# Performance work log

Hardware: AMD Instinct MI355X
Metric: run time of the kernel (lower is better)

## Reference

```python
import jax, jax.numpy as jnp
import numpy as np

# Ragged layout: 8 sequences packed into total_tokens=6144 tokens.
_SEQLENS = [1024, 512, 1024, 256, 768, 1024, 512, 1024]
_TOTAL = sum(_SEQLENS)  # 6144
_H, _D = 16, 128
_MAXLEN = 1024


def setup_inputs() -> dict:
    key = jax.random.key(0)
    kq, kk, kv = jax.random.split(key, 3)
    cu = jnp.asarray(np.concatenate([[0], np.cumsum(_SEQLENS)]), dtype=jnp.int32)
    return {
        "q": jax.random.normal(kq, (_TOTAL, _H, _D), dtype=jnp.float32),
        "k": jax.random.normal(kk, (_TOTAL, _H, _D), dtype=jnp.float32),
        "v": jax.random.normal(kv, (_TOTAL, _H, _D), dtype=jnp.float32),
        "cu_seqlens_q": cu,
        "cu_seqlens_k": cu,
        "max_seqlen_q": _MAXLEN,
        "max_seqlen_k": _MAXLEN,
    }


def _pad_gather(x, cu, L):
    """Gather packed [T,h,d] into padded [B,L,h,d] plus validity mask [B,L]."""
    starts = cu[:-1]                                   # [B]
    lens = cu[1:] - cu[:-1]                            # [B]
    pos = jnp.arange(L, dtype=cu.dtype)                # [L]
    idx = starts[:, None] + pos[None, :]               # [B,L]
    mask = pos[None, :] < lens[:, None]                # [B,L]
    idx = jnp.clip(idx, 0, x.shape[0] - 1)
    return x[idx], mask, jnp.where(mask, idx, x.shape[0])


def reference(q, k, v, cu_seqlens_q, cu_seqlens_k, max_seqlen_q, max_seqlen_k):
    # Equivalent to pytorch_varlen_attention: per-sequence SDPA (non-causal,
    # no dropout), vectorized via pad-to-max + key masking.
    T, h, d = q.shape
    qp, mq, idx_q = _pad_gather(q, cu_seqlens_q, max_seqlen_q)  # [B,Lq,h,d]
    kp, mk, _ = _pad_gather(k, cu_seqlens_k, max_seqlen_k)      # [B,Lk,h,d]
    vp, _, _ = _pad_gather(v, cu_seqlens_k, max_seqlen_k)

    scale = 1.0 / jnp.sqrt(jnp.asarray(d, dtype=q.dtype))
    scores = jnp.einsum("bqhd,bkhd->bhqk", qp, kp) * scale      # [B,h,Lq,Lk]
    neg = jnp.asarray(jnp.finfo(scores.dtype).min, scores.dtype)
    scores = jnp.where(mk[:, None, None, :], scores, neg)
    attn = jax.nn.softmax(scores, axis=-1)
    out_pad = jnp.einsum("bhqk,bkhd->bqhd", attn, vp)           # [B,Lq,h,d]

    # Scatter valid rows back to packed layout; invalid rows dropped (idx==T).
    out = jnp.zeros((T, h, d), dtype=q.dtype)
    out = out.at[idx_q.reshape(-1)].set(
        out_pad.reshape(-1, h, d), mode="drop")
    return out
```

## Files before the change

### kernel.cpp

```cpp
#include <hip/hip_runtime.h>
#include <hip/hip_bf16.h>
#include <stdint.h>

#define H 16
#define D 128
#define BM 256
#define BN 64
#define NW 8
#define NT 512

typedef __bf16 bf16_t;
typedef bf16_t bf16x8 __attribute__((ext_vector_type(8)));
typedef bf16_t bf16x2 __attribute__((ext_vector_type(2)));
typedef float f32x16 __attribute__((ext_vector_type(16)));

#define MFMA32(a, b, c) __builtin_amdgcn_mfma_f32_32x32x16_bf16(a, b, c, 0, 0, 0)

union FragU { uint32_t w[4]; bf16x8 v; };

static __device__ __forceinline__ uint32_t cvtpk_bf16(float lo, float hi) {
  uint32_t r;
  asm("v_cvt_pk_bf16_f32 %0, %1, %2" : "=v"(r) : "v"(lo), "v"(hi));
  return r;
}

static __device__ __forceinline__ void gld_lds16(const bf16_t* g, bf16_t* l) {
  __builtin_amdgcn_global_load_lds(
      (const __attribute__((address_space(1))) void*)g,
      (__attribute__((address_space(3))) void*)l, 16, 0, 0);
}

static __device__ __forceinline__ float xhalf(float v, int hi) {
  uint32_t b = __builtin_bit_cast(uint32_t, v);
  auto p = __builtin_amdgcn_permlane32_swap(b, b, false, false);
  uint32_t o = hi ? p[0] : p[1];
  return __builtin_bit_cast(float, o);
}


__global__ void conv_k(const float* __restrict__ kin, bf16_t* __restrict__ kb, int n8) {
  int i = blockIdx.x * blockDim.x + threadIdx.x;
  int stride = gridDim.x * blockDim.x;
  for (; i < n8; i += stride) {
    const float* p = kin + (size_t)i * 8;
    float4 a = *(const float4*)p, b = *(const float4*)(p + 4);
    bf16x8 w;
    w[0] = (bf16_t)a.x; w[1] = (bf16_t)a.y; w[2] = (bf16_t)a.z; w[3] = (bf16_t)a.w;
    w[4] = (bf16_t)b.x; w[5] = (bf16_t)b.y; w[6] = (bf16_t)b.z; w[7] = (bf16_t)b.w;
    *(bf16x8*)(kb + (size_t)i * 8) = w;
  }
}

__global__ void conv_vt(const float* __restrict__ v, bf16_t* __restrict__ vt,
                        const int* __restrict__ cuk, int nseq) {
  int tile = blockIdx.x, h = blockIdx.y;
  int acc = 0, seq = -1, lt = 0, s0k = 0, Lk = 0, Lkp = 0;
  size_t vb = 0;
  for (int s = 0; s < nseq; ++s) {
    int Ls = cuk[s + 1] - cuk[s];
    int Lp = (Ls + 63) & ~63;
    int nt = Lp / 64;
    if (tile < acc + nt) { seq = s; lt = tile - acc; s0k = cuk[s]; Lk = Ls; Lkp = Lp; break; }
    acc += nt; vb += (size_t)H * D * Lp;
  }
  if (seq < 0) return;
  int kv0 = lt * 64;
  int d = threadIdx.x;
  bf16x8 w[8];
  #pragma unroll
  for (int j = 0; j < 64; ++j) {
    int kv = kv0 + j;
    int kvc = kv < Lk ? kv : Lk - 1;
    float val = v[((size_t)(s0k + kvc) * H + h) * D + d];
    w[j >> 3][j & 7] = (bf16_t)val;
  }
  bf16_t* dstT = vt + vb + (size_t)h * D * Lkp + (size_t)lt * 8192;
  #pragma unroll
  for (int c = 0; c < 8; ++c)
    *(bf16x8*)(dstT + ((size_t)c * 128 + d) * 8) = w[c];
}


__global__ __launch_bounds__(NT, 2)
void fa_varlen15(const float* __restrict__ q,
                 const bf16_t* __restrict__ kb,
                 const bf16_t* __restrict__ vt,
                 const int* __restrict__ cuq,
                 const int* __restrict__ cuk,
                 float* __restrict__ out,
                 int nseq, int maxtiles)
{
  __shared__ alignas(16) bf16_t sK[2][BN * D];
  __shared__ alignas(16) bf16_t sVt[3][8 * 128 * 8];

  const int nwg = gridDim.x;
  const int orig = blockIdx.x;
  const int qq = nwg >> 3, rr = nwg & 7;
  const int xcd = orig & 7;
  const int wgid = (xcd < rr ? xcd * (qq + 1) : rr * (qq + 1) + (xcd - rr) * qq) + (orig >> 3);
  const int tile = wgid % maxtiles;
  const int h = wgid / maxtiles;

  int acc = 0, seq = -1, lt = 0, s0q = 0, s0k = 0, Lq = 0, Lk = 0, Lkp = 0;
  size_t vb = 0;
  for (int s = 0; s < nseq; ++s) {
    int a = cuq[s], b = cuq[s + 1];
    int Ls = b - a;
    int nt = (Ls + BM - 1) / BM;
    int Lks = cuk[s + 1] - cuk[s];
    int Lp = (Lks + 63) & ~63;
    if (tile < acc + nt) {
      seq = s; lt = tile - acc; s0q = a; Lq = Ls;
      s0k = cuk[s]; Lk = Lks; Lkp = Lp;
      break;
    }
    acc += nt; vb += (size_t)H * D * Lp;
  }
  if (seq < 0) return;

  const int q0 = lt * BM;
  const int tid = threadIdx.x;
  const int lane = tid & 63;
  const int lq = lane & 31;
  const int hi = lane >> 5;

  const float SC = 0.08838834764831845f * 1.44269504088896340f;

  bf16x8 qf[8];
  {
    int warp = tid >> 6;
    int qrow = q0 + warp * 32 + lq; if (qrow >= Lq) qrow = Lq - 1;
    const float* qp = q + ((size_t)(s0q + qrow) * H + h) * D;
    #pragma unroll
    for (int ks = 0; ks < 8; ++ks) {
      const float* p = qp + ks * 16 + hi * 8;
      float4 a = *(const float4*)p, b = *(const float4*)(p + 4);
      bf16x8 r;
      r[0] = (bf16_t)(a.x * SC); r[1] = (bf16_t)(a.y * SC);
      r[2] = (bf16_t)(a.z * SC); r[3] = (bf16_t)(a.w * SC);
      r[4] = (bf16_t)(b.x * SC); r[5] = (bf16_t)(b.y * SC);
      r[6] = (bf16_t)(b.z * SC); r[7] = (bf16_t)(b.w * SC);
      qf[ks] = r;
    }
  }

  const bf16_t* vsrcH = vt + vb + (size_t)h * D * Lkp;

  auto STAGE_K = [&](int tt, int buf) {
    const int kvb = tt * BN;
    #pragma unroll
    for (int i = 0; i < 2; ++i) {
      int g = tid + i * NT;
      int row = g >> 4, cc = g & 15;
      int kvr = kvb + row; if (kvr >= Lk) kvr = Lk - 1;
      const bf16_t* src = kb + ((size_t)(s0k + kvr) * H + h) * D + ((cc ^ (row & 7)) << 3);
      gld_lds16(src, &sK[buf][g * 8]);
    }
  };
  auto STAGE_V = [&](int tt, int buf) {
    const bf16_t* vsrc = vsrcH + (size_t)tt * 8192;
    #pragma unroll
    for (int i = 0; i < 2; ++i) {
      int g = tid + i * NT;
      gld_lds16(vsrc + (size_t)g * 8, &sVt[buf][g * 8]);
    }
  };

  f32x16 oacc[4];
  #pragma unroll
  for (int dt = 0; dt < 4; ++dt)
    #pragma unroll
    for (int r = 0; r < 16; ++r) oacc[dt][r] = 0.f;
  float m = -1e30f, l = 0.f;

  FragU paP, pbP;
  #pragma unroll
  for (int i = 0; i < 4; ++i) { paP.w[i] = 0u; pbP.w[i] = 0u; }
  float alphaP = 1.0f;
  int tP = 0, ctP = 0;

  const int nkv = (Lk + BN - 1) / BN;

  STAGE_K(0, 0);
  STAGE_V(0, 0);
  asm volatile("s_waitcnt vmcnt(0)" ::: "memory");
  __builtin_amdgcn_s_barrier();
  __builtin_amdgcn_sched_barrier(0);

  for (int t = 0; t < nkv; ++t) {
    const int kvb = t * BN;
    int tn = t + 1 < nkv ? t + 1 : nkv - 1;
    STAGE_K(tn, (t + 1) & 1);
    STAGE_V(tn, (t + 1) % 3);

    const bf16_t* sKc = sK[t & 1];
    const bool tail = (kvb + BN > Lk);

    #pragma unroll
    for (int ct = 0; ct < 2; ++ct) {
      f32x16 sa, sb;
      #pragma unroll
      for (int r = 0; r < 16; ++r) { sa[r] = 0.f; sb[r] = 0.f; }
      int krow = ct * 32 + lq;
      __builtin_amdgcn_s_setprio(1);
      #pragma unroll
      for (int ks = 0; ks < 4; ++ks) {
        int posa = (ks * 2 + hi) ^ (krow & 7);
        bf16x8 kfa = *(const bf16x8*)&sKc[krow * 128 + (posa << 3)];
        sa = MFMA32(kfa, qf[ks], sa);
        int posb = ((ks + 4) * 2 + hi) ^ (krow & 7);
        bf16x8 kfb = *(const bf16x8*)&sKc[krow * 128 + (posb << 3)];
        sb = MFMA32(kfb, qf[ks + 4], sb);
      }
      __builtin_amdgcn_s_setprio(0);

      if (__any(alphaP != 1.0f)) {
        #pragma unroll
        for (int r = 0; r < 16; ++r) {
          int cr = (r & 3) + 8 * (r >> 2) + 4 * hi;
          float a2 = __shfl(alphaP, cr);
          #pragma unroll
          for (int dt = 0; dt < 4; ++dt) oacc[dt][r] *= a2;
        }
      }
      {
        const bf16_t* sVp = sVt[tP % 3];
        #pragma unroll
        for (int dt = 0; dt < 4; ++dt) {
          int drow = dt * 32 + lq;
          bf16x8 vf0 = *(const bf16x8*)&sVp[((ctP * 4 + hi) * 128 + drow) << 3];
          oacc[dt] = MFMA32(paP.v, vf0, oacc[dt]);
          bf16x8 vf1 = *(const bf16x8*)&sVp[((ctP * 4 + 2 + hi) * 128 + drow) << 3];
          oacc[dt] = MFMA32(pbP.v, vf1, oacc[dt]);
        }
      }

      f32x16 st;
      #pragma unroll
      for (int r = 0; r < 16; ++r) {
        float x = sa[r] + sb[r];
        if (tail) {
          int kvi = kvb + ct * 32 + (r & 3) + 8 * (r >> 2) + 4 * hi;
          if (kvi >= Lk) x = -1e30f;
        }
        st[r] = x;
      }
      float m0;
      {
        float a0 = fmaxf(st[0], st[1]),  a1 = fmaxf(st[2], st[3]);
        float a2 = fmaxf(st[4], st[5]),  a3 = fmaxf(st[6], st[7]);
        float a4 = fmaxf(st[8], st[9]),  a5 = fmaxf(st[10], st[11]);
        float a6 = fmaxf(st[12], st[13]), a7 = fmaxf(st[14], st[15]);
        float b0 = fmaxf(a0, a1), b1 = fmaxf(a2, a3);
        float b2 = fmaxf(a4, a5), b3 = fmaxf(a6, a7);
        m0 = fmaxf(fmaxf(b0, b1), fmaxf(b2, b3));
      }
      float m1 = fmaxf(m0, xhalf(m0, hi));
      bool trig = m1 > m + 8.0f;
      float mnew = trig ? m1 : m;
      float alpha = __builtin_amdgcn_exp2f(m - mnew);
      m = mnew;

      #pragma unroll
      for (int r = 0; r < 16; ++r)
        st[r] = __builtin_amdgcn_exp2f(st[r] - m);
      float psum;
      {
        float a0 = st[0] + st[1],  a1 = st[2] + st[3];
        float a2 = st[4] + st[5],  a3 = st[6] + st[7];
        float a4 = st[8] + st[9],  a5 = st[10] + st[11];
        float a6 = st[12] + st[13], a7 = st[14] + st[15];
        float b0 = a0 + a1, b1 = a2 + a3, b2 = a4 + a5, b3 = a6 + a7;
        psum = (b0 + b1) + (b2 + b3);
      }
      psum += xhalf(psum, hi);
      l = l * alpha + psum;

      uint32_t c0 = cvtpk_bf16(st[0],  st[1]),  c1 = cvtpk_bf16(st[2],  st[3]);
      uint32_t c2 = cvtpk_bf16(st[4],  st[5]),  c3 = cvtpk_bf16(st[6],  st[7]);
      uint32_t c4 = cvtpk_bf16(st[8],  st[9]),  c5 = cvtpk_bf16(st[10], st[11]);
      uint32_t c6 = cvtpk_bf16(st[12], st[13]), c7 = cvtpk_bf16(st[14], st[15]);
      { auto rr2 = __builtin_amdgcn_permlane32_swap(c0, c2, false, false); c0 = rr2[0]; c2 = rr2[1]; }
      { auto rr2 = __builtin_amdgcn_permlane32_swap(c1, c3, false, false); c1 = rr2[0]; c3 = rr2[1]; }
      { auto rr2 = __builtin_amdgcn_permlane32_swap(c4, c6, false, false); c4 = rr2[0]; c6 = rr2[1]; }
      { auto rr2 = __builtin_amdgcn_permlane32_swap(c5, c7, false, false); c5 = rr2[0]; c7 = rr2[1]; }
      paP.w[0] = c0; paP.w[1] = c1; paP.w[2] = c2; paP.w[3] = c3;
      pbP.w[0] = c4; pbP.w[1] = c5; pbP.w[2] = c6; pbP.w[3] = c7;
      alphaP = alpha; tP = t; ctP = ct;
    }

    asm volatile("s_waitcnt vmcnt(2)" ::: "memory");
    __builtin_amdgcn_s_barrier();
    __builtin_amdgcn_sched_barrier(0);
  }

  if (__any(alphaP != 1.0f)) {
    #pragma unroll
    for (int r = 0; r < 16; ++r) {
      int cr = (r & 3) + 8 * (r >> 2) + 4 * hi;
      float a2 = __shfl(alphaP, cr);
      #pragma unroll
      for (int dt = 0; dt < 4; ++dt) oacc[dt][r] *= a2;
    }
  }
  {
    const bf16_t* sVp = sVt[tP % 3];
    #pragma unroll
    for (int dt = 0; dt < 4; ++dt) {
      int drow = dt * 32 + lq;
      bf16x8 vf0 = *(const bf16x8*)&sVp[((ctP * 4 + hi) * 128 + drow) << 3];
      oacc[dt] = MFMA32(paP.v, vf0, oacc[dt]);
      bf16x8 vf1 = *(const bf16x8*)&sVp[((ctP * 4 + 2 + hi) * 128 + drow) << 3];
      oacc[dt] = MFMA32(pbP.v, vf1, oacc[dt]);
    }
  }

  #pragma unroll
  for (int r = 0; r < 16; ++r) {
    int cr = (r & 3) + 8 * (r >> 2) + 4 * hi;
    int warp = tid >> 6;
    int qr = q0 + warp * 32 + cr;
    float lcr = __shfl(l, cr);
    if (qr < Lq) {
      float rn = 1.0f / lcr;
      float* op = out + ((size_t)(s0q + qr) * H + h) * D + lq;
      #pragma unroll
      for (int dt = 0; dt < 4; ++dt)
        op[dt * 32] = oacc[dt][r] * rn;
    }
  }
}


__global__ __launch_bounds__(256, 3)
void fa_varlen2(const float* __restrict__ q,
                const float* __restrict__ k,
                const float* __restrict__ v,
                const int* __restrict__ cuq,
                const int* __restrict__ cuk,
                float* __restrict__ out,
                int nseq)
{
  __shared__ alignas(16) bf16_t sBuf[128 * 128];
  __shared__ float sRed[4 * 32];
  bf16_t* sK  = sBuf;
  bf16_t* sVt = sBuf + 64 * 128;

  const int tile = blockIdx.x;
  const int h = blockIdx.y;

  int acc = 0, seq = -1, lt = 0, s0q = 0, s0k = 0, Lq = 0, Lk = 0;
  for (int s = 0; s < nseq; ++s) {
    int a = cuq[s], b = cuq[s + 1];
    int Ls = b - a;
    int nt = (Ls + 127) / 128;
    if (tile < acc + nt) {
      seq = s; lt = tile - acc; s0q = a; Lq = Ls;
      s0k = cuk[s]; Lk = cuk[s + 1] - s0k;
      break;
    }
    acc += nt;
  }
  if (seq < 0) return;

  const int q0 = lt * 128;
  const int tid = threadIdx.x;
  const int warp = tid >> 6;
  const int lane = tid & 63;
  const int lq = lane & 31;
  const int hi = lane >> 5;

  const float SC = 0.08838834764831845f * 1.44269504088896340f;

  #pragma unroll
  for (int ii = 0; ii < 8; ++ii) {
    int g = tid + ii * 256;
    int row = g >> 4, cc = g & 15;
    int gr = q0 + row; if (gr >= Lq) gr = Lq - 1;
    const float* p = q + ((size_t)(s0q + gr) * H + h) * D + cc * 8;
    float4 f0 = *(const float4*)p;
    float4 f1 = *(const float4*)(p + 4);
    bf16x8 w;
    w[0] = (bf16_t)f0.x; w[1] = (bf16_t)f0.y; w[2] = (bf16_t)f0.z; w[3] = (bf16_t)f0.w;
    w[4] = (bf16_t)f1.x; w[5] = (bf16_t)f1.y; w[6] = (bf16_t)f1.z; w[7] = (bf16_t)f1.w;
    *(bf16x8*)&sBuf[row * 128 + (((cc ^ (row & 7))) << 3)] = w;
  }
  __syncthreads();

  bf16x8 qf[8];
  {
    int row = warp * 32 + lq;
    #pragma unroll
    for (int ks = 0; ks < 8; ++ks) {
      int pos = (ks * 2 + hi) ^ (row & 7);
      qf[ks] = *(const bf16x8*)&sBuf[row * 128 + (pos << 3)];
    }
  }

  f32x16 oacc[4];
  #pragma unroll
  for (int dt = 0; dt < 4; ++dt)
    #pragma unroll
    for (int r = 0; r < 16; ++r) oacc[dt][r] = 0.f;
  float m = -1e30f, l = 0.f;

  const int nkv = (Lk + 63) / 64;
  for (int it = 0; it < nkv; ++it) {
    const int kv0 = it * 64;
    __syncthreads();

    #pragma unroll
    for (int ii = 0; ii < 4; ++ii) {
      int g = tid + ii * 256;
      int row = g >> 4, cc = g & 15;
      int gr = kv0 + row; if (gr >= Lk) gr = Lk - 1;
      const float* p = k + ((size_t)(s0k + gr) * H + h) * D + cc * 8;
      float4 f0 = *(const float4*)p;
      float4 f1 = *(const float4*)(p + 4);
      bf16x8 w;
      w[0] = (bf16_t)f0.x; w[1] = (bf16_t)f0.y; w[2] = (bf16_t)f0.z; w[3] = (bf16_t)f0.w;
      w[4] = (bf16_t)f1.x; w[5] = (bf16_t)f1.y; w[6] = (bf16_t)f1.z; w[7] = (bf16_t)f1.w;
      *(bf16x8*)&sK[row * 128 + (((cc ^ (row & 7))) << 3)] = w;
    }
    {
      int kp = tid & 31;
      int seg = tid >> 5;
      int r0 = kv0 + 2 * kp, r1 = r0 + 1;
      if (r0 >= Lk) r0 = Lk - 1;
      if (r1 >= Lk) r1 = Lk - 1;
      const float* p0 = v + ((size_t)(s0k + r0) * H + h) * D + seg * 16;
      const float* p1 = v + ((size_t)(s0k + r1) * H + h) * D + seg * 16;
      float va[16], vbf[16];
      *(float4*)&va[0]  = *(const float4*)p0;
      *(float4*)&va[4]  = *(const float4*)(p0 + 4);
      *(float4*)&va[8]  = *(const float4*)(p0 + 8);
      *(float4*)&va[12] = *(const float4*)(p0 + 12);
      *(float4*)&vbf[0]  = *(const float4*)p1;
      *(float4*)&vbf[4]  = *(const float4*)(p1 + 4);
      *(float4*)&vbf[8]  = *(const float4*)(p1 + 8);
      *(float4*)&vbf[12] = *(const float4*)(p1 + 12);
      int kvr = 2 * kp;
      #pragma unroll
      for (int i = 0; i < 16; ++i) {
        int d = seg * 16 + i;
        int pos = (kp >> 2) ^ (d & 7);
        bf16x2 w2; w2[0] = (bf16_t)va[i]; w2[1] = (bf16_t)vbf[i];
        *(bf16x2*)&sVt[d * 64 + (pos << 3) + (kvr & 7)] = w2;
      }
    }
    __syncthreads();

    const bool tail = (kv0 + 64 > Lk);

    #pragma unroll
    for (int ct = 0; ct < 2; ++ct) {
      f32x16 st;
      #pragma unroll
      for (int r = 0; r < 16; ++r) st[r] = 0.f;
      int krow = ct * 32 + lq;
      #pragma unroll
      for (int ks = 0; ks < 8; ++ks) {
        int pos = (ks * 2 + hi) ^ (krow & 7);
        bf16x8 kf = *(const bf16x8*)&sK[krow * 128 + (pos << 3)];
        st = MFMA32(kf, qf[ks], st);
      }

      float tmax = -1e30f;
      #pragma unroll
      for (int r = 0; r < 16; ++r) {
        float x = st[r] * SC;
        if (tail) {
          int kvi = kv0 + ct * 32 + (r & 3) + 8 * (r >> 2) + 4 * hi;
          if (kvi >= Lk) x = -1e30f;
        }
        st[r] = x;
        tmax = fmaxf(tmax, x);
      }
      tmax = fmaxf(tmax, __shfl_xor(tmax, 32));
      bool trig = tmax > m + 8.0f;
      float mnew = trig ? tmax : m;
      float alpha = exp2f(m - mnew);
      m = mnew;

      float psum = 0.f;
      #pragma unroll
      for (int r = 0; r < 16; ++r) {
        float e = exp2f(st[r] - m);
        st[r] = e;
        psum += e;
      }
      psum += __shfl_xor(psum, 32);
      l = l * alpha + psum;

      if (__any(alpha != 1.0f)) {
        if (hi == 0) sRed[warp * 32 + lq] = alpha;
        asm volatile("s_waitcnt lgkmcnt(0)" ::: "memory");
        #pragma unroll
        for (int r = 0; r < 16; ++r) {
          float a2 = sRed[warp * 32 + (r & 3) + 8 * (r >> 2) + 4 * hi];
          #pragma unroll
          for (int dt = 0; dt < 4; ++dt) oacc[dt][r] *= a2;
        }
      }

      uint32_t c0 = cvtpk_bf16(st[0],  st[1]),  c1 = cvtpk_bf16(st[2],  st[3]);
      uint32_t c2 = cvtpk_bf16(st[4],  st[5]),  c3 = cvtpk_bf16(st[6],  st[7]);
      uint32_t c4 = cvtpk_bf16(st[8],  st[9]),  c5 = cvtpk_bf16(st[10], st[11]);
      uint32_t c6 = cvtpk_bf16(st[12], st[13]), c7 = cvtpk_bf16(st[14], st[15]);
      { auto rr2 = __builtin_amdgcn_permlane32_swap(c0, c2, false, false); c0 = rr2[0]; c2 = rr2[1]; }
      { auto rr2 = __builtin_amdgcn_permlane32_swap(c1, c3, false, false); c1 = rr2[0]; c3 = rr2[1]; }
      { auto rr2 = __builtin_amdgcn_permlane32_swap(c4, c6, false, false); c4 = rr2[0]; c6 = rr2[1]; }
      { auto rr2 = __builtin_amdgcn_permlane32_swap(c5, c7, false, false); c5 = rr2[0]; c7 = rr2[1]; }
      FragU pa, pb;
      pa.w[0] = c0; pa.w[1] = c1; pa.w[2] = c2; pa.w[3] = c3;
      pb.w[0] = c4; pb.w[1] = c5; pb.w[2] = c6; pb.w[3] = c7;

      #pragma unroll
      for (int dt = 0; dt < 4; ++dt) {
        int drow = dt * 32 + lq;
        int pos0 = (ct * 4 + hi) ^ (drow & 7);
        bf16x8 vf0 = *(const bf16x8*)&sVt[drow * 64 + (pos0 << 3)];
        oacc[dt] = MFMA32(pa.v, vf0, oacc[dt]);
        int pos1 = (ct * 4 + 2 + hi) ^ (drow & 7);
        bf16x8 vf1 = *(const bf16x8*)&sVt[drow * 64 + (pos1 << 3)];
        oacc[dt] = MFMA32(pb.v, vf1, oacc[dt]);
      }
    }
  }

  if (hi == 0) sRed[warp * 32 + lq] = l;
  asm volatile("s_waitcnt lgkmcnt(0)" ::: "memory");
  #pragma unroll
  for (int r = 0; r < 16; ++r) {
    int cr = (r & 3) + 8 * (r >> 2) + 4 * hi;
    int qr = q0 + warp * 32 + cr;
    if (qr < Lq) {
      float rn = 1.0f / sRed[warp * 32 + cr];
      float* op = out + ((size_t)(s0q + qr) * H + h) * D + lq;
      #pragma unroll
      for (int dt = 0; dt < 4; ++dt)
        op[dt * 32] = oacc[dt][r] * rn;
    }
  }
}

extern "C" void kernel_launch(void* const* d_in, const int* in_sizes, int n_in,
                              void* d_out, int out_size, void* d_ws, size_t ws_size,
                              hipStream_t stream) {
  const float* q = (const float*)d_in[0];
  const float* k = (const float*)d_in[1];
  const float* v = (const float*)d_in[2];
  const int* cuq = (const int*)d_in[3];
  const int* cuk = (const int*)d_in[4];
  float* out = (float*)d_out;

  int total = in_sizes[0] / (H * D);
  int nseq = in_sizes[3] - 1;
  int maxtiles = (total + BM - 1) / BM + nseq;

  size_t needK = (size_t)in_sizes[1] * 2;
  size_t needV = (size_t)in_sizes[2] * 2 + (size_t)nseq * 64 * H * D * 2 + 256;

  if (ws_size >= needK + needV) {
    bf16_t* kb = (bf16_t*)d_ws;
    bf16_t* vtb = (bf16_t*)((char*)d_ws + needK);

    conv_k<<<1024, 256, 0, stream>>>(k, kb, in_sizes[1] / 8);
    int maxvt = (total + 63) / 64 + nseq;
    dim3 gvt(maxvt, H);
    conv_vt<<<gvt, 128, 0, stream>>>(v, vtb, cuk, nseq);
    fa_varlen15<<<dim3(maxtiles * H), NT, 0, stream>>>(q, kb, vtb, cuq, cuk, out, nseq, maxtiles);
  } else {
    int mt2 = (total + 127) / 128 + nseq;
    dim3 grid(mt2, H);
    fa_varlen2<<<grid, 256, 0, stream>>>(q, k, v, cuq, cuk, out, nseq);
  }
}
```

Before: 122.4 us.

## Split long-sequence KV range into two chunks with a combine kernel

Adds a split-KV attention kernel. Q tiles of sequences with more than 8 KV tiles are processed by two workgroups, each covering half of the KV range and writing partial outputs plus row max and sum to workspace. A separate combine kernel then merges the two halves. This gives more workgroups and better load balance across CUs for the ragged batch. The cost is an extra launch, bf16 partial-output traffic with some precision loss, and a larger workspace requirement. The old fp32-input fallback kernel is removed.

```diff
diff --git a/kernel.cpp b/kernel.cpp
--- a/kernel.cpp
+++ b/kernel.cpp
@@ -6,12 +6,10 @@
 #define D 128
 #define BM 256
 #define BN 64
-#define NW 8
 #define NT 512
 
 typedef __bf16 bf16_t;
 typedef bf16_t bf16x8 __attribute__((ext_vector_type(8)));
-typedef bf16_t bf16x2 __attribute__((ext_vector_type(2)));
 typedef float f32x16 __attribute__((ext_vector_type(16)));
 
 #define MFMA32(a, b, c) __builtin_amdgcn_mfma_f32_32x32x16_bf16(a, b, c, 0, 0, 0)
@@ -78,6 +76,344 @@
   #pragma unroll
   for (int c = 0; c < 8; ++c)
     *(bf16x8*)(dstT + ((size_t)c * 128 + d) * 8) = w[c];
+}
+
+
+__global__ __launch_bounds__(NT, 2)
+void fa_split(const float* __restrict__ q,
+              const bf16_t* __restrict__ kb,
+              const bf16_t* __restrict__ vt,
+              const int* __restrict__ cuq,
+              const int* __restrict__ cuk,
+              float* __restrict__ out,
+              bf16_t* __restrict__ pO,
+              float* __restrict__ pm,
+              float* __restrict__ pl,
+              int nseq, int maxt, int upb)
+{
+  __shared__ alignas(16) bf16_t sK[2][BN * D];
+  __shared__ alignas(16) bf16_t sVt[3][8 * 128 * 8];
+
+  const int nwg = gridDim.x;
+  const int orig = blockIdx.x;
+  const int qq = nwg >> 3, rr = nwg & 7;
+  const int xcd = orig & 7;
+  const int wgid = (xcd < rr ? xcd * (qq + 1) : rr * (qq + 1) + (xcd - rr) * qq) + (orig >> 3);
+  const int u = wgid % upb;
+  const int h = wgid / upb;
+
+  int accU = 0, accT = 0, seq = -1, qtile = 0, chunk = 0, tileIdx = 0;
+  int s0q = 0, s0k = 0, Lq = 0, Lk = 0, Lkp = 0, nkv = 0, cs = 1;
+  size_t vb = 0;
+  for (int s = 0; s < nseq; ++s) {
+    int a = cuq[s], b = cuq[s + 1];
+    int Ls = b - a;
+    int nt = (Ls + BM - 1) / BM;
+    int Lks = cuk[s + 1] - cuk[s];
+    int Lp = (Lks + 63) & ~63;
+    int nk = (Lks + 63) / 64;
+    int c2 = nk > 8 ? 2 : 1;
+    if (u < accU + nt * c2) {
+      int local = u - accU;
+      seq = s; chunk = local / nt; qtile = local % nt; tileIdx = accT + qtile;
+      s0q = a; Lq = Ls; s0k = cuk[s]; Lk = Lks; Lkp = Lp; nkv = nk; cs = c2;
+      break;
+    }
+    accU += nt * c2; accT += nt; vb += (size_t)H * D * Lp;
+  }
+  if (seq < 0) return;
+
+  const int t0 = chunk * 8;
+  const int t1 = (chunk == 0) ? (nkv < 8 ? nkv : 8) : nkv;
+
+  const int q0 = qtile * BM;
+  const int tid = threadIdx.x;
+  const int lane = tid & 63;
+  const int lq = lane & 31;
+  const int hi = lane >> 5;
+  const int warp = tid >> 6;
+
+  const float SC = 0.08838834764831845f * 1.44269504088896340f;
+
+  bf16x8 qf[8];
+  {
+    int qrow = q0 + warp * 32 + lq; if (qrow >= Lq) qrow = Lq - 1;
+    const float* qp = q + ((size_t)(s0q + qrow) * H + h) * D;
+    #pragma unroll
+    for (int ks = 0; ks < 8; ++ks) {
+      const float* p = qp + ks * 16 + hi * 8;
+      float4 a = *(const float4*)p, b = *(const float4*)(p + 4);
+      bf16x8 r;
+      r[0] = (bf16_t)(a.x * SC); r[1] = (bf16_t)(a.y * SC);
+      r[2] = (bf16_t)(a.z * SC); r[3] = (bf16_t)(a.w * SC);
+      r[4] = (bf16_t)(b.x * SC); r[5] = (bf16_t)(b.y * SC);
+      r[6] = (bf16_t)(b.z * SC); r[7] = (bf16_t)(b.w * SC);
+      qf[ks] = r;
+    }
+  }
+
+  const bf16_t* vsrcH = vt + vb + (size_t)h * D * Lkp;
+
+  auto STAGE_K = [&](int tt, int buf) {
+    const int kvb = tt * BN;
+    #pragma unroll
+    for (int i = 0; i < 2; ++i) {
+      int g = tid + i * NT;
+      int row = g >> 4, cc = g & 15;
+      int kvr = kvb + row; if (kvr >= Lk) kvr = Lk - 1;
+      const bf16_t* src = kb + ((size_t)(s0k + kvr) * H + h) * D + ((cc ^ (row & 7)) << 3);
+      gld_lds16(src, &sK[buf][g * 8]);
+    }
+  };
+  auto STAGE_V = [&](int tt, int buf) {
+    const bf16_t* vsrc = vsrcH + (size_t)tt * 8192;
+    #pragma unroll
+    for (int i = 0; i < 2; ++i) {
+      int g = tid + i * NT;
+      gld_lds16(vsrc + (size_t)g * 8, &sVt[buf][g * 8]);
+    }
+  };
+
+  f32x16 oacc[4];
+  #pragma unroll
+  for (int dt = 0; dt < 4; ++dt)
+    #pragma unroll
+    for (int r = 0; r < 16; ++r) oacc[dt][r] = 0.f;
+  float m = -1e30f, l = 0.f;
+
+  FragU paP, pbP;
+  #pragma unroll
+  for (int i = 0; i < 4; ++i) { paP.w[i] = 0u; pbP.w[i] = 0u; }
+  float alphaP = 1.0f;
+  int tP = t0, ctP = 0;
+
+  STAGE_K(t0, t0 & 1);
+  STAGE_V(t0, t0 % 3);
+  asm volatile("s_waitcnt vmcnt(0)" ::: "memory");
+  __builtin_amdgcn_s_barrier();
+  __builtin_amdgcn_sched_barrier(0);
+
+  for (int t = t0; t < t1; ++t) {
+    const int kvb = t * BN;
+    int tn = t + 1 < t1 ? t + 1 : t1 - 1;
+    STAGE_K(tn, (t + 1) & 1);
+    STAGE_V(tn, (t + 1) % 3);
+
+    const bf16_t* sKc = sK[t & 1];
+    const bool tail = (kvb + BN > Lk);
+
+    #pragma unroll
+    for (int ct = 0; ct < 2; ++ct) {
+      f32x16 sa, sb;
+      #pragma unroll
+      for (int r = 0; r < 16; ++r) { sa[r] = 0.f; sb[r] = 0.f; }
+      int krow = ct * 32 + lq;
+      __builtin_amdgcn_s_setprio(1);
+      #pragma unroll
+      for (int ks = 0; ks < 4; ++ks) {
+        int posa = (ks * 2 + hi) ^ (krow & 7);
+        bf16x8 kfa = *(const bf16x8*)&sKc[krow * 128 + (posa << 3)];
+        sa = MFMA32(kfa, qf[ks], sa);
+        int posb = ((ks + 4) * 2 + hi) ^ (krow & 7);
+        bf16x8 kfb = *(const bf16x8*)&sKc[krow * 128 + (posb << 3)];
+        sb = MFMA32(kfb, qf[ks + 4], sb);
+      }
+      __builtin_amdgcn_s_setprio(0);
+
+      if (__any(alphaP != 1.0f)) {
+        #pragma unroll
+        for (int r = 0; r < 16; ++r) {
+          int cr = (r & 3) + 8 * (r >> 2) + 4 * hi;
+          float a2 = __shfl(alphaP, cr);
+          #pragma unroll
+          for (int dt = 0; dt < 4; ++dt) oacc[dt][r] *= a2;
+        }
+      }
+      {
+        const bf16_t* sVp = sVt[tP % 3];
+        #pragma unroll
+        for (int dt = 0; dt < 4; ++dt) {
+          int drow = dt * 32 + lq;
+          bf16x8 vf0 = *(const bf16x8*)&sVp[((ctP * 4 + hi) * 128 + drow) << 3];
+          oacc[dt] = MFMA32(paP.v, vf0, oacc[dt]);
+          bf16x8 vf1 = *(const bf16x8*)&sVp[((ctP * 4 + 2 + hi) * 128 + drow) << 3];
+          oacc[dt] = MFMA32(pbP.v, vf1, oacc[dt]);
+        }
+      }
+
+      f32x16 st;
+      #pragma unroll
+      for (int r = 0; r < 16; ++r) {
+        float x = sa[r] + sb[r];
+        if (tail) {
+          int kvi = kvb + ct * 32 + (r & 3) + 8 * (r >> 2) + 4 * hi;
+          if (kvi >= Lk) x = -1e30f;
+        }
+        st[r] = x;
+      }
+      float m0;
+      {
+        float a0 = fmaxf(st[0], st[1]),  a1 = fmaxf(st[2], st[3]);
+        float a2 = fmaxf(st[4], st[5]),  a3 = fmaxf(st[6], st[7]);
+        float a4 = fmaxf(st[8], st[9]),  a5 = fmaxf(st[10], st[11]);
+        float a6 = fmaxf(st[12], st[13]), a7 = fmaxf(st[14], st[15]);
+        float b0 = fmaxf(a0, a1), b1 = fmaxf(a2, a3);
+        float b2 = fmaxf(a4, a5), b3 = fmaxf(a6, a7);
+        m0 = fmaxf(fmaxf(b0, b1), fmaxf(b2, b3));
+      }
+      float m1 = fmaxf(m0, xhalf(m0, hi));
+      bool trig = m1 > m + 8.0f;
+      float mnew = trig ? m1 : m;
+      float alpha = __builtin_amdgcn_exp2f(m - mnew);
+      m = mnew;
+
+      #pragma unroll
+      for (int r = 0; r < 16; ++r)
+        st[r] = __builtin_amdgcn_exp2f(st[r] - m);
+      float psum;
+      {
+        float a0 = st[0] + st[1],  a1 = st[2] + st[3];
+        float a2 = st[4] + st[5],  a3 = st[6] + st[7];
+        float a4 = st[8] + st[9],  a5 = st[10] + st[11];
+        float a6 = st[12] + st[13], a7 = st[14] + st[15];
+        float b0 = a0 + a1, b1 = a2 + a3, b2 = a4 + a5, b3 = a6 + a7;
+        psum = (b0 + b1) + (b2 + b3);
+      }
+      psum += xhalf(psum, hi);
+      l = l * alpha + psum;
+
+      uint32_t c0 = cvtpk_bf16(st[0],  st[1]),  c1 = cvtpk_bf16(st[2],  st[3]);
+      uint32_t c2 = cvtpk_bf16(st[4],  st[5]),  c3 = cvtpk_bf16(st[6],  st[7]);
+      uint32_t c4 = cvtpk_bf16(st[8],  st[9]),  c5 = cvtpk_bf16(st[10], st[11]);
+      uint32_t c6 = cvtpk_bf16(st[12], st[13]), c7 = cvtpk_bf16(st[14], st[15]);
+      { auto w2 = __builtin_amdgcn_permlane32_swap(c0, c2, false, false); c0 = w2[0]; c2 = w2[1]; }
+      { auto w2 = __builtin_amdgcn_permlane32_swap(c1, c3, false, false); c1 = w2[0]; c3 = w2[1]; }
+      { auto w2 = __builtin_amdgcn_permlane32_swap(c4, c6, false, false); c4 = w2[0]; c6 = w2[1]; }
+      { auto w2 = __builtin_amdgcn_permlane32_swap(c5, c7, false, false); c5 = w2[0]; c7 = w2[1]; }
+      paP.w[0] = c0; paP.w[1] = c1; paP.w[2] = c2; paP.w[3] = c3;
+      pbP.w[0] = c4; pbP.w[1] = c5; pbP.w[2] = c6; pbP.w[3] = c7;
+      alphaP = alpha; tP = t; ctP = ct;
+    }
+
+    asm volatile("s_waitcnt vmcnt(2)" ::: "memory");
+    __builtin_amdgcn_s_barrier();
+    __builtin_amdgcn_sched_barrier(0);
+  }
+
+  if (__any(alphaP != 1.0f)) {
+    #pragma unroll
+    for (int r = 0; r < 16; ++r) {
+      int cr = (r & 3) + 8 * (r >> 2) + 4 * hi;
+      float a2 = __shfl(alphaP, cr);
+      #pragma unroll
+      for (int dt = 0; dt < 4; ++dt) oacc[dt][r] *= a2;
+    }
+  }
+  {
+    const bf16_t* sVp = sVt[tP % 3];
+    #pragma unroll
+    for (int dt = 0; dt < 4; ++dt) {
+      int drow = dt * 32 + lq;
+      bf16x8 vf0 = *(const bf16x8*)&sVp[((ctP * 4 + hi) * 128 + drow) << 3];
+      oacc[dt] = MFMA32(paP.v, vf0, oacc[dt]);
+      bf16x8 vf1 = *(const bf16x8*)&sVp[((ctP * 4 + 2 + hi) * 128 + drow) << 3];
+      oacc[dt] = MFMA32(pbP.v, vf1, oacc[dt]);
+    }
+  }
+
+  if (cs == 2) {
+    const size_t slot = (size_t)(h * maxt + tileIdx) * 2 + chunk;
+    bf16_t* po = pO + slot * (256 * 128);
+    #pragma unroll
+    for (int r = 0; r < 16; ++r) {
+      int cr = (r & 3) + 8 * (r >> 2) + 4 * hi;
+      int row = warp * 32 + cr;
+      #pragma unroll
+      for (int dt = 0; dt < 4; ++dt)
+        po[row * 128 + dt * 32 + lq] = (bf16_t)oacc[dt][r];
+    }
+    if (hi == 0) {
+      pm[slot * 256 + warp * 32 + lq] = m;
+      pl[slot * 256 + warp * 32 + lq] = l;
+    }
+  } else {
+    #pragma unroll
+    for (int r = 0; r < 16; ++r) {
+      int cr = (r & 3) + 8 * (r >> 2) + 4 * hi;
+      int qr = q0 + warp * 32 + cr;
+      float lcr = __shfl(l, cr);
+      if (qr < Lq) {
+        float rn = 1.0f / lcr;
+        float* op = out + ((size_t)(s0q + qr) * H + h) * D + lq;
+        #pragma unroll
+        for (int dt = 0; dt < 4; ++dt)
+          op[dt * 32] = oacc[dt][r] * rn;
+      }
+    }
+  }
+}
+
+
+__global__ __launch_bounds__(256)
+void fa_combine(const int* __restrict__ cuq, const int* __restrict__ cuk,
+                const bf16_t* __restrict__ pO, const float* __restrict__ pm,
+                const float* __restrict__ pl, float* __restrict__ out,
+                int nseq, int maxt)
+{
+  int gt = blockIdx.x >> 2;
+  int rg = blockIdx.x & 3;
+  int h = gt / maxt;
+  int tileIdx = gt % maxt;
+
+  int accT = 0, seq = -1, qtile = 0, s0q = 0, Lq = 0, nkv = 0;
+  for (int s = 0; s < nseq; ++s) {
+    int a = cuq[s], b = cuq[s + 1];
+    int Ls = b - a;
+    int nt = (Ls + BM - 1) / BM;
+    if (tileIdx < accT + nt) {
+      seq = s; qtile = tileIdx - accT; s0q = a; Lq = Ls;
+      nkv = (cuk[s + 1] - cuk[s] + 63) / 64;
+      break;
+    }
+    accT += nt;
+  }
+  if (seq < 0 || nkv <= 8) return;
+
+  int tid = threadIdx.x;
+  int row = rg * 64 + (tid >> 2);
+  int dbase = (tid & 3) * 32;
+  int qr = qtile * BM + row;
+  if (qr >= Lq) return;
+
+  size_t s0 = (size_t)(h * maxt + tileIdx) * 2;
+  size_t s1 = s0 + 1;
+  float m0 = pm[s0 * 256 + row], l0 = pl[s0 * 256 + row];
+  float m1 = pm[s1 * 256 + row], l1 = pl[s1 * 256 + row];
+  float M = fmaxf(m0, m1);
+  float w0 = __builtin_amdgcn_exp2f(m0 - M);
+  float w1 = __builtin_amdgcn_exp2f(m1 - M);
+  float rn = 1.0f / (w0 * l0 + w1 * l1);
+  w0 *= rn; w1 *= rn;
+
+  const bf16_t* p0 = pO + s0 * (256 * 128) + row * 128 + dbase;
+  const bf16_t* p1 = pO + s1 * (256 * 128) + row * 128 + dbase;
+  float* op = out + ((size_t)(s0q + qr) * H + h) * D + dbase;
+  #pragma unroll
+  for (int j = 0; j < 4; ++j) {
+    bf16x8 a = *(const bf16x8*)(p0 + j * 8);
+    bf16x8 b = *(const bf16x8*)(p1 + j * 8);
+    float4 o0, o1;
+    o0.x = w0 * (float)a[0] + w1 * (float)b[0];
+    o0.y = w0 * (float)a[1] + w1 * (float)b[1];
+    o0.z = w0 * (float)a[2] + w1 * (float)b[2];
+    o0.w = w0 * (float)a[3] + w1 * (float)b[3];
+    o1.x = w0 * (float)a[4] + w1 * (float)b[4];
+    o1.y = w0 * (float)a[5] + w1 * (float)b[5];
+    o1.z = w0 * (float)a[6] + w1 * (float)b[6];
+    o1.w = w0 * (float)a[7] + w1 * (float)b[7];
+    *(float4*)(op + j * 8) = o0;
+    *(float4*)(op + j * 8 + 4) = o1;
+  }
 }
 
 
@@ -123,12 +459,12 @@
   const int lane = tid & 63;
   const int lq = lane & 31;
   const int hi = lane >> 5;
+  const int warp = tid >> 6;
 
   const float SC = 0.08838834764831845f * 1.44269504088896340f;
 
   bf16x8 qf[8];
   {
-    int warp = tid >> 6;
     int qrow = q0 + warp * 32 + lq; if (qrow >= Lq) qrow = Lq - 1;
     const float* qp = q + ((size_t)(s0q + qrow) * H + h) * D;
     #pragma unroll
@@ -280,10 +616,10 @@
       uint32_t c2 = cvtpk_bf16(st[4],  st[5]),  c3 = cvtpk_bf16(st[6],  st[7]);
       uint32_t c4 = cvtpk_bf16(st[8],  st[9]),  c5 = cvtpk_bf16(st[10], st[11]);
       uint32_t c6 = cvtpk_bf16(st[12], st[13]), c7 = cvtpk_bf16(st[14], st[15]);
-      { auto rr2 = __builtin_amdgcn_permlane32_swap(c0, c2, false, false); c0 = rr2[0]; c2 = rr2[1]; }
-      { auto rr2 = __builtin_amdgcn_permlane32_swap(c1, c3, false, false); c1 = rr2[0]; c3 = rr2[1]; }
-      { auto rr2 = __builtin_amdgcn_permlane32_swap(c4, c6, false, false); c4 = rr2[0]; c6 = rr2[1]; }
-      { auto rr2 = __builtin_amdgcn_permlane32_swap(c5, c7, false, false); c5 = rr2[0]; c7 = rr2[1]; }
+      { auto w2 = __builtin_amdgcn_permlane32_swap(c0, c2, false, false); c0 = w2[0]; c2 = w2[1]; }
+      { auto w2 = __builtin_amdgcn_permlane32_swap(c1, c3, false, false); c1 = w2[0]; c3 = w2[1]; }
+      { auto w2 = __builtin_amdgcn_permlane32_swap(c4, c6, false, false); c4 = w2[0]; c6 = w2[1]; }
+      { auto w2 = __builtin_amdgcn_permlane32_swap(c5, c7, false, false); c5 = w2[0]; c7 = w2[1]; }
       paP.w[0] = c0; paP.w[1] = c1; paP.w[2] = c2; paP.w[3] = c3;
       pbP.w[0] = c4; pbP.w[1] = c5; pbP.w[2] = c6; pbP.w[3] = c7;
       alphaP = alpha; tP = t; ctP = ct;
@@ -318,224 +654,10 @@
   #pragma unroll
   for (int r = 0; r < 16; ++r) {
     int cr = (r & 3) + 8 * (r >> 2) + 4 * hi;
-    int warp = tid >> 6;
     int qr = q0 + warp * 32 + cr;
     float lcr = __shfl(l, cr);
     if (qr < Lq) {
       float rn = 1.0f / lcr;
-      float* op = out + ((size_t)(s0q + qr) * H + h) * D + lq;
-      #pragma unroll
-      for (int dt = 0; dt < 4; ++dt)
-        op[dt * 32] = oacc[dt][r] * rn;
-    }
-  }
-}
-
-
-__global__ __launch_bounds__(256, 3)
-void fa_varlen2(const float* __restrict__ q,
-                const float* __restrict__ k,
-                const float* __restrict__ v,
-                const int* __restrict__ cuq,
-                const int* __restrict__ cuk,
-                float* __restrict__ out,
-                int nseq)
-{
-  __shared__ alignas(16) bf16_t sBuf[128 * 128];
-  __shared__ float sRed[4 * 32];
-  bf16_t* sK  = sBuf;
-  bf16_t* sVt = sBuf + 64 * 128;
-
-  const int tile = blockIdx.x;
-  const int h = blockIdx.y;
-
-  int acc = 0, seq = -1, lt = 0, s0q = 0, s0k = 0, Lq = 0, Lk = 0;
-  for (int s = 0; s < nseq; ++s) {
-    int a = cuq[s], b = cuq[s + 1];
-    int Ls = b - a;
-    int nt = (Ls + 127) / 128;
-    if (tile < acc + nt) {
-      seq = s; lt = tile - acc; s0q = a; Lq = Ls;
-      s0k = cuk[s]; Lk = cuk[s + 1] - s0k;
-      break;
-    }
-    acc += nt;
-  }
-  if (seq < 0) return;
-
-  const int q0 = lt * 128;
-  const int tid = threadIdx.x;
-  const int warp = tid >> 6;
-  const int lane = tid & 63;
-  const int lq = lane & 31;
-  const int hi = lane >> 5;
-
-  const float SC = 0.08838834764831845f * 1.44269504088896340f;
-
-  #pragma unroll
-  for (int ii = 0; ii < 8; ++ii) {
-    int g = tid + ii * 256;
-    int row = g >> 4, cc = g & 15;
-    int gr = q0 + row; if (gr >= Lq) gr = Lq - 1;
-    const float* p = q + ((size_t)(s0q + gr) * H + h) * D + cc * 8;
-    float4 f0 = *(const float4*)p;
-    float4 f1 = *(const float4*)(p + 4);
-    bf16x8 w;
-    w[0] = (bf16_t)f0.x; w[1] = (bf16_t)f0.y; w[2] = (bf16_t)f0.z; w[3] = (bf16_t)f0.w;
-    w[4] = (bf16_t)f1.x; w[5] = (bf16_t)f1.y; w[6] = (bf16_t)f1.z; w[7] = (bf16_t)f1.w;
-    *(bf16x8*)&sBuf[row * 128 + (((cc ^ (row & 7))) << 3)] = w;
-  }
-  __syncthreads();
-
-  bf16x8 qf[8];
-  {
-    int row = warp * 32 + lq;
-    #pragma unroll
-    for (int ks = 0; ks < 8; ++ks) {
-      int pos = (ks * 2 + hi) ^ (row & 7);
-      qf[ks] = *(const bf16x8*)&sBuf[row * 128 + (pos << 3)];
-    }
-  }
-
-  f32x16 oacc[4];
-  #pragma unroll
-  for (int dt = 0; dt < 4; ++dt)
-    #pragma unroll
-    for (int r = 0; r < 16; ++r) oacc[dt][r] = 0.f;
-  float m = -1e30f, l = 0.f;
-
-  const int nkv = (Lk + 63) / 64;
-  for (int it = 0; it < nkv; ++it) {
-    const int kv0 = it * 64;
-    __syncthreads();
-
-    #pragma unroll
-    for (int ii = 0; ii < 4; ++ii) {
-      int g = tid + ii * 256;
-      int row = g >> 4, cc = g & 15;
-      int gr = kv0 + row; if (gr >= Lk) gr = Lk - 1;
-      const float* p = k + ((size_t)(s0k + gr) * H + h) * D + cc * 8;
-      float4 f0 = *(const float4*)p;
-      float4 f1 = *(const float4*)(p + 4);
-      bf16x8 w;
-      w[0] = (bf16_t)f0.x; w[1] = (bf16_t)f0.y; w[2] = (bf16_t)f0.z; w[3] = (bf16_t)f0.w;
-      w[4] = (bf16_t)f1.x; w[5] = (bf16_t)f1.y; w[6] = (bf16_t)f1.z; w[7] = (bf16_t)f1.w;
-      *(bf16x8*)&sK[row * 128 + (((cc ^ (row & 7))) << 3)] = w;
-    }
-    {
-      int kp = tid & 31;
-      int seg = tid >> 5;
-      int r0 = kv0 + 2 * kp, r1 = r0 + 1;
-      if (r0 >= Lk) r0 = Lk - 1;
-      if (r1 >= Lk) r1 = Lk - 1;
-      const float* p0 = v + ((size_t)(s0k + r0) * H + h) * D + seg * 16;
-      const float* p1 = v + ((size_t)(s0k + r1) * H + h) * D + seg * 16;
-      float va[16], vbf[16];
-      *(float4*)&va[0]  = *(const float4*)p0;
-      *(float4*)&va[4]  = *(const float4*)(p0 + 4);
-      *(float4*)&va[8]  = *(const float4*)(p0 + 8);
-      *(float4*)&va[12] = *(const float4*)(p0 + 12);
-      *(float4*)&vbf[0]  = *(const float4*)p1;
-      *(float4*)&vbf[4]  = *(const float4*)(p1 + 4);
-      *(float4*)&vbf[8]  = *(const float4*)(p1 + 8);
-      *(float4*)&vbf[12] = *(const float4*)(p1 + 12);
-      int kvr = 2 * kp;
-      #pragma unroll
-      for (int i = 0; i < 16; ++i) {
-        int d = seg * 16 + i;
-        int pos = (kp >> 2) ^ (d & 7);
-        bf16x2 w2; w2[0] = (bf16_t)va[i]; w2[1] = (bf16_t)vbf[i];
-        *(bf16x2*)&sVt[d * 64 + (pos << 3) + (kvr & 7)] = w2;
-      }
-    }
-    __syncthreads();
-
-    const bool tail = (kv0 + 64 > Lk);
-
-    #pragma unroll
-    for (int ct = 0; ct < 2; ++ct) {
-      f32x16 st;
-      #pragma unroll
-      for (int r = 0; r < 16; ++r) st[r] = 0.f;
-      int krow = ct * 32 + lq;
-      #pragma unroll
-      for (int ks = 0; ks < 8; ++ks) {
-        int pos = (ks * 2 + hi) ^ (krow & 7);
-        bf16x8 kf = *(const bf16x8*)&sK[krow * 128 + (pos << 3)];
-        st = MFMA32(kf, qf[ks], st);
-      }
-
-      float tmax = -1e30f;
-      #pragma unroll
-      for (int r = 0; r < 16; ++r) {
-        float x = st[r] * SC;
-        if (tail) {
-          int kvi = kv0 + ct * 32 + (r & 3) + 8 * (r >> 2) + 4 * hi;
-          if (kvi >= Lk) x = -1e30f;
-        }
-        st[r] = x;
-        tmax = fmaxf(tmax, x);
-      }
-      tmax = fmaxf(tmax, __shfl_xor(tmax, 32));
-      bool trig = tmax > m + 8.0f;
-      float mnew = trig ? tmax : m;
-      float alpha = exp2f(m - mnew);
-      m = mnew;
-
-      float psum = 0.f;
-      #pragma unroll
-      for (int r = 0; r < 16; ++r) {
-        float e = exp2f(st[r] - m);
-        st[r] = e;
-        psum += e;
-      }
-      psum += __shfl_xor(psum, 32);
-      l = l * alpha + psum;
-
-      if (__any(alpha != 1.0f)) {
-        if (hi == 0) sRed[warp * 32 + lq] = alpha;
-        asm volatile("s_waitcnt lgkmcnt(0)" ::: "memory");
-        #pragma unroll
-        for (int r = 0; r < 16; ++r) {
-          float a2 = sRed[warp * 32 + (r & 3) + 8 * (r >> 2) + 4 * hi];
-          #pragma unroll
-          for (int dt = 0; dt < 4; ++dt) oacc[dt][r] *= a2;
-        }
-      }
-
-      uint32_t c0 = cvtpk_bf16(st[0],  st[1]),  c1 = cvtpk_bf16(st[2],  st[3]);
-      uint32_t c2 = cvtpk_bf16(st[4],  st[5]),  c3 = cvtpk_bf16(st[6],  st[7]);
-      uint32_t c4 = cvtpk_bf16(st[8],  st[9]),  c5 = cvtpk_bf16(st[10], st[11]);
-      uint32_t c6 = cvtpk_bf16(st[12], st[13]), c7 = cvtpk_bf16(st[14], st[15]);
-      { auto rr2 = __builtin_amdgcn_permlane32_swap(c0, c2, false, false); c0 = rr2[0]; c2 = rr2[1]; }
-      { auto rr2 = __builtin_amdgcn_permlane32_swap(c1, c3, false, false); c1 = rr2[0]; c3 = rr2[1]; }
-      { auto rr2 = __builtin_amdgcn_permlane32_swap(c4, c6, false, false); c4 = rr2[0]; c6 = rr2[1]; }
-      { auto rr2 = __builtin_amdgcn_permlane32_swap(c5, c7, false, false); c5 = rr2[0]; c7 = rr2[1]; }
-      FragU pa, pb;
-      pa.w[0] = c0; pa.w[1] = c1; pa.w[2] = c2; pa.w[3] = c3;
-      pb.w[0] = c4; pb.w[1] = c5; pb.w[2] = c6; pb.w[3] = c7;
-
-      #pragma unroll
-      for (int dt = 0; dt < 4; ++dt) {
-        int drow = dt * 32 + lq;
-        int pos0 = (ct * 4 + hi) ^ (drow & 7);
-        bf16x8 vf0 = *(const bf16x8*)&sVt[drow * 64 + (pos0 << 3)];
-        oacc[dt] = MFMA32(pa.v, vf0, oacc[dt]);
-        int pos1 = (ct * 4 + 2 + hi) ^ (drow & 7);
-        bf16x8 vf1 = *(const bf16x8*)&sVt[drow * 64 + (pos1 << 3)];
-        oacc[dt] = MFMA32(pb.v, vf1, oacc[dt]);
-      }
-    }
-  }
-
-  if (hi == 0) sRed[warp * 32 + lq] = l;
-  asm volatile("s_waitcnt lgkmcnt(0)" ::: "memory");
-  #pragma unroll
-  for (int r = 0; r < 16; ++r) {
-    int cr = (r & 3) + 8 * (r >> 2) + 4 * hi;
-    int qr = q0 + warp * 32 + cr;
-    if (qr < Lq) {
-      float rn = 1.0f / sRed[warp * 32 + cr];
       float* op = out + ((size_t)(s0q + qr) * H + h) * D + lq;
       #pragma unroll
       for (int dt = 0; dt < 4; ++dt)
@@ -556,23 +678,35 @@
 
   int total = in_sizes[0] / (H * D);
   int nseq = in_sizes[3] - 1;
-  int maxtiles = (total + BM - 1) / BM + nseq;
+  int maxt = (total + BM - 1) / BM + nseq;
+  int upb = 2 * maxt;
 
   size_t needK = (size_t)in_sizes[1] * 2;
   size_t needV = (size_t)in_sizes[2] * 2 + (size_t)nseq * 64 * H * D * 2 + 256;
-
-  if (ws_size >= needK + needV) {
+  size_t slots = (size_t)maxt * H * 2;
+  size_t needPO = slots * 256 * 128 * 2;
+  size_t needML = slots * 256 * 4 * 2;
+
+  if (ws_size >= needK + needV + needPO + needML + 256) {
     bf16_t* kb = (bf16_t*)d_ws;
     bf16_t* vtb = (bf16_t*)((char*)d_ws + needK);
+    bf16_t* pO = (bf16_t*)((char*)d_ws + needK + needV);
+    float* pm = (float*)((char*)d_ws + needK + needV + needPO);
+    float* pl = pm + slots * 256;
 
     conv_k<<<1024, 256, 0, stream>>>(k, kb, in_sizes[1] / 8);
     int maxvt = (total + 63) / 64 + nseq;
-    dim3 gvt(maxvt, H);
-    conv_vt<<<gvt, 128, 0, stream>>>(v, vtb, cuk, nseq);
-    fa_varlen15<<<dim3(maxtiles * H), NT, 0, stream>>>(q, kb, vtb, cuq, cuk, out, nseq, maxtiles);
-  } else {
-    int mt2 = (total + 127) / 128 + nseq;
-    dim3 grid(mt2, H);
-    fa_varlen2<<<grid, 256, 0, stream>>>(q, k, v, cuq, cuk, out, nseq);
-  }
-}
+    conv_vt<<<dim3(maxvt, H), 128, 0, stream>>>(v, vtb, cuk, nseq);
+    fa_split<<<dim3(upb * H), NT, 0, stream>>>(q, kb, vtb, cuq, cuk, out,
+                                               pO, pm, pl, nseq, maxt, upb);
+    fa_combine<<<dim3(maxt * H * 4), 256, 0, stream>>>(cuq, cuk, pO, pm, pl,
+                                                       out, nseq, maxt);
+  } else if (ws_size >= needK + needV) {
+    bf16_t* kb = (bf16_t*)d_ws;
+    bf16_t* vtb = (bf16_t*)((char*)d_ws + needK);
+    conv_k<<<1024, 256, 0, stream>>>(k, kb, in_sizes[1] / 8);
+    int maxvt = (total + 63) / 64 + nseq;
+    conv_vt<<<dim3(maxvt, H), 128, 0, stream>>>(v, vtb, cuk, nseq);
+    fa_varlen15<<<dim3(maxt * H), NT, 0, stream>>>(q, kb, vtb, cuq, cuk, out, nseq, maxt);
+  }
+}
```

Result: slower. 145.6 us (+18.9%).
